# Kernel tuning notes

Measured on AMD Instinct MI355X. Metric: run time of the kernel, lower is better.

## Reference

```python
import jax, jax.numpy as jnp
import numpy as np
import math

D_MODEL = 1024
H = 16
D_K = D_MODEL // H
D_FF = 4096
NEG = -1e9


def layer_norm(x, alpha, bias):
    # Faithful to source: mean over last dim, UNBIASED std (torch.std default),
    # eps defined in source but never used in forward.
    mean = jnp.mean(x, axis=-1, keepdims=True)
    std = jnp.std(x, axis=-1, ddof=1, keepdims=True)
    return (x - mean) / std * alpha + bias


def mha(x, mask, w_q, w_k, w_v, w_o):
    B, S, D = x.shape
    q = (x @ w_q.T).reshape(B, S, H, D_K)
    k = (x @ w_k.T).reshape(B, S, H, D_K)
    v = (x @ w_v.T).reshape(B, S, H, D_K)
    scores = jnp.einsum('bqhd,bkhd->bhqk', q, k) / math.sqrt(D_K)
    scores = jnp.where(mask, NEG, scores)
    attn = jax.nn.softmax(scores, axis=-1)
    out = jnp.einsum('bhqk,bkhd->bqhd', attn, v).reshape(B, S, D)
    return out @ w_o.T


def setup_inputs() -> dict:
    key = jax.random.key(0)
    ks = jax.random.split(key, 16)
    B, S = 4, 2048
    s = 0.02
    return {
        'x': jax.random.normal(ks[0], (B, S, D_MODEL), jnp.float32),
        'w_q': jax.random.normal(ks[1], (D_MODEL, D_MODEL), jnp.float32) * s,
        'w_k': jax.random.normal(ks[2], (D_MODEL, D_MODEL), jnp.float32) * s,
        'w_v': jax.random.normal(ks[3], (D_MODEL, D_MODEL), jnp.float32) * s,
        'w_o': jax.random.normal(ks[4], (D_MODEL, D_MODEL), jnp.float32) * s,
        'l1_w': jax.random.normal(ks[5], (D_FF, D_MODEL), jnp.float32) * s,
        'l1_b': jnp.zeros((D_FF,), jnp.float32),
        'l2_w': jax.random.normal(ks[6], (D_MODEL, D_FF), jnp.float32) * s,
        'l2_b': jnp.zeros((D_MODEL,), jnp.float32),
        'norm1_a': jnp.ones((D_MODEL,), jnp.float32),
        'norm1_b': jnp.zeros((D_MODEL,), jnp.float32),
        'norm2_a': jnp.ones((D_MODEL,), jnp.float32),
        'norm2_b': jnp.zeros((D_MODEL,), jnp.float32),
        'normf_a': jnp.ones((D_MODEL,), jnp.float32),
        'normf_b': jnp.zeros((D_MODEL,), jnp.float32),
        'mask': jax.random.randint(ks[7], (B, 1, 1, S), 0, 2) == 1,
    }


def reference(x, w_q, w_k, w_v, w_o, l1_w, l1_b, l2_w, l2_b,
              norm1_a, norm1_b, norm2_a, norm2_b, normf_a, normf_b, mask):
    # residual 1: pre-norm self-attention (dropout is identity at eval)
    x = x + mha(layer_norm(x, norm1_a, norm1_b), mask, w_q, w_k, w_v, w_o)
    # residual 2: pre-norm FFN
    h = layer_norm(x, norm2_a, norm2_b)
    ff = jax.nn.relu(h @ l1_w.T + l1_b) @ l2_w.T + l2_b
    x = x + ff
    return layer_norm(x, normf_a, normf_b)
```

## Files before the change

### kernel.cpp

```cpp
#include <hip/hip_runtime.h>
#include <hip/hip_bf16.h>


typedef __bf16 bf16x8 __attribute__((ext_vector_type(8)));
typedef float f32x4 __attribute__((ext_vector_type(4)));
typedef unsigned short u16x8 __attribute__((ext_vector_type(8)));
using bf16 = __hip_bfloat16;

__device__ __forceinline__ f32x4 mfma16(bf16x8 a, bf16x8 b, f32x4 c) {
  return __builtin_amdgcn_mfma_f32_16x16x32_bf16(a, b, c, 0, 0, 0);
}

__device__ __forceinline__ int swz(int row, int blk) {
  return row * 64 + ((blk ^ (row & 7)) << 3);
}

__device__ __forceinline__ void stage_tile64(unsigned short* lds,
                                             const bf16* g, int ld, int rows) {
  const int lane = threadIdx.x & 63, wid = threadIdx.x >> 6;
  const int r8 = lane >> 3, blk = lane & 7;
  const bf16* gl = g + (size_t)r8 * ld + ((blk ^ r8) << 3);
  const int passes = rows >> 3;
  for (int p = wid; p < passes; p += 4) {
    __builtin_amdgcn_global_load_lds(
        (const __attribute__((address_space(1))) void*)(gl + (size_t)(p * 8) * ld),
        (__attribute__((address_space(3))) void*)(lds + p * 512),
        16, 0, 0);
  }
}

__device__ __forceinline__ void stage_half512(unsigned short* lds,
                                              const bf16* g, int ld) {
  const int lane = threadIdx.x & 63, w8 = threadIdx.x >> 6;
  const int r8 = lane >> 3, blk = lane & 7;
  const bf16* gl = g + (size_t)r8 * ld + ((blk ^ r8) << 3);
  __builtin_amdgcn_global_load_lds(
      (const __attribute__((address_space(1))) void*)(gl + (size_t)(w8 * 8) * ld),
      (__attribute__((address_space(3))) void*)(lds + w8 * 512), 16, 0, 0);
  __builtin_amdgcn_global_load_lds(
      (const __attribute__((address_space(1))) void*)(gl + (size_t)((w8 + 8) * 8) * ld),
      (__attribute__((address_space(3))) void*)(lds + (w8 + 8) * 512), 16, 0, 0);
}

__device__ __forceinline__ short bfb(float x) {
  return (short)__hip_bfloat16_raw(__float2bfloat16(x)).x;
}

__global__ __launch_bounds__(256) void cvt_k(const float* __restrict__ s,
                                             bf16* __restrict__ d, int n) {
  const int i = (blockIdx.x * 256 + threadIdx.x) * 4;
  if (i + 3 < n) {
    const float4 v = *reinterpret_cast<const float4*>(s + i);
    ushort4 o;
    o.x = (unsigned short)bfb(v.x);
    o.y = (unsigned short)bfb(v.y);
    o.z = (unsigned short)bfb(v.z);
    o.w = (unsigned short)bfb(v.w);
    *reinterpret_cast<ushort4*>(d + i) = o;
  }
}

template <bool OUT_F32>
__global__ __launch_bounds__(256) void layernorm_k(const float* __restrict__ in,
                                                   const float* __restrict__ gamma,
                                                   const float* __restrict__ beta,
                                                   void* __restrict__ out) {
  __shared__ float red[8];
  const int row = blockIdx.x, t = threadIdx.x;
  const float4 vv = reinterpret_cast<const float4*>(in + (size_t)row * 1024)[t];
  const float x0 = vv.x, x1 = vv.y, x2 = vv.z, x3 = vv.w;
  float s = x0 + x1 + x2 + x3;
#pragma unroll
  for (int off = 32; off; off >>= 1) s += __shfl_down(s, off);
  if ((t & 63) == 0) red[t >> 6] = s;
  __syncthreads();
  const float mean = (red[0] + red[1] + red[2] + red[3]) * (1.0f / 1024.0f);
  const float d0 = x0 - mean, d1 = x1 - mean, d2 = x2 - mean, d3 = x3 - mean;
  float sq = d0 * d0 + d1 * d1 + d2 * d2 + d3 * d3;
#pragma unroll
  for (int off = 32; off; off >>= 1) sq += __shfl_down(sq, off);
  if ((t & 63) == 0) red[4 + (t >> 6)] = sq;
  __syncthreads();
  const float var =
      fmaxf((red[4] + red[5] + red[6] + red[7]) * (1.0f / 1023.0f), 1e-20f);
  const float rstd = rsqrtf(var);
  const float4 ga = reinterpret_cast<const float4*>(gamma)[t];
  const float4 be = reinterpret_cast<const float4*>(beta)[t];
  const float y0 = d0 * rstd * ga.x + be.x;
  const float y1 = d1 * rstd * ga.y + be.y;
  const float y2 = d2 * rstd * ga.z + be.z;
  const float y3 = d3 * rstd * ga.w + be.w;
  if (OUT_F32) {
    reinterpret_cast<float4*>((float*)out + (size_t)row * 1024)[t] =
        make_float4(y0, y1, y2, y3);
  } else {
    ushort4 o;
    o.x = (unsigned short)bfb(y0);
    o.y = (unsigned short)bfb(y1);
    o.z = (unsigned short)bfb(y2);
    o.w = (unsigned short)bfb(y3);
    reinterpret_cast<ushort4*>((bf16*)out + (size_t)row * 1024)[t] = o;
  }
}

template <bool HAS_BIAS, bool RELU, bool HAS_RES, bool OUT_F32>
__global__ __launch_bounds__(256) void gemm_bt(const bf16* __restrict__ A,
                                               const bf16* __restrict__ W,
                                               const float* __restrict__ bias,
                                               const float* __restrict__ resid,
                                               void* __restrict__ out,
                                               int M, int N, int K,
                                               int lda, int ldw) {
  __shared__ __align__(16) unsigned short As[128 * 64];
  __shared__ __align__(16) unsigned short Bs[128 * 64];
  const int lane = threadIdx.x & 63, wid = threadIdx.x >> 6;
  const int n16 = lane & 15, quad = lane >> 4;
  const int wm = (wid >> 1) * 64, wn = (wid & 1) * 64;
  const int tm = blockIdx.x * 128, tn = blockIdx.y * 128;
  f32x4 acc[4][4] = {};
  for (int k0 = 0; k0 < K; k0 += 64) {
    stage_tile64(As, A + (size_t)tm * lda + k0, lda, 128);
    stage_tile64(Bs, W + (size_t)tn * ldw + k0, ldw, 128);
    __syncthreads();
#pragma unroll
    for (int kk = 0; kk < 64; kk += 32) {
      bf16x8 af[4], bw[4];
#pragma unroll
      for (int i = 0; i < 4; ++i)
        af[i] = *reinterpret_cast<const bf16x8*>(
            &As[swz(wm + i * 16 + n16, (kk >> 3) + quad)]);
#pragma unroll
      for (int j = 0; j < 4; ++j)
        bw[j] = *reinterpret_cast<const bf16x8*>(
            &Bs[swz(wn + j * 16 + n16, (kk >> 3) + quad)]);
#pragma unroll
      for (int i = 0; i < 4; ++i)
#pragma unroll
        for (int j = 0; j < 4; ++j) acc[i][j] = mfma16(af[i], bw[j], acc[i][j]);
    }
    __syncthreads();
  }
#pragma unroll
  for (int i = 0; i < 4; ++i) {
#pragma unroll
    for (int j = 0; j < 4; ++j) {
      const int n = tn + wn + j * 16 + n16;
      const float bv = HAS_BIAS ? bias[n] : 0.0f;
#pragma unroll
      for (int r = 0; r < 4; ++r) {
        const int m = tm + wm + i * 16 + quad * 4 + r;
        float vv = acc[i][j][r] + bv;
        if (RELU) vv = fmaxf(vv, 0.0f);
        if (HAS_RES) vv += resid[(size_t)m * N + n];
        if (OUT_F32)
          ((float*)out)[(size_t)m * N + n] = vv;
        else
          ((bf16*)out)[(size_t)m * N + n] = __float2bfloat16(vv);
      }
    }
  }
}

#define PHASE2(BUFSEL, QB, DO_B, STAGES, WAITS)                                \
  {                                                                            \
    const unsigned short* LA = Lds + (BUFSEL)*32768 + lasel * 8192;            \
    if (DO_B) {                                                                \
      const unsigned short* LB =                                               \
          Lds + (BUFSEL)*32768 + 16384 + lbsel * 8192;                         \
      _Pragma("unroll") for (int j = 0; j < 4; ++j) {                          \
        const int br = bloc + j * 16 + n16;                                    \
        bfr[j][0] = *reinterpret_cast<const bf16x8*>(&LB[swz(br, quad)]);      \
        bfr[j][1] = *reinterpret_cast<const bf16x8*>(&LB[swz(br, 4 + quad)]);  \
      }                                                                        \
    }                                                                          \
    bf16x8 a0[4], a1[4];                                                       \
    _Pragma("unroll") for (int ii = 0; ii < 4; ++ii) {                         \
      const int ar = ((QB)*2 + ii) * 16 + n16;                                 \
      a0[ii] = *reinterpret_cast<const bf16x8*>(&LA[swz(ar, quad)]);           \
      a1[ii] = *reinterpret_cast<const bf16x8*>(&LA[swz(ar, 4 + quad)]);       \
    }                                                                          \
    STAGES;                                                                    \
    WAITS;                                                                     \
    __builtin_amdgcn_sched_barrier(0);                                         \
    __builtin_amdgcn_s_barrier();                                              \
    asm volatile("s_waitcnt lgkmcnt(0)" ::: "memory");                         \
    __builtin_amdgcn_sched_barrier(0);                                         \
    __builtin_amdgcn_s_setprio(1);                                             \
    _Pragma("unroll") for (int ii = 0; ii < 4; ++ii)                           \
        _Pragma("unroll") for (int j = 0; j < 4; ++j) {                        \
      f32x4 c = acc[(QB)*2 + ii][j];                                           \
      c = mfma16(a0[ii], bfr[j][0], c);                                        \
      c = mfma16(a1[ii], bfr[j][1], c);                                        \
      acc[(QB)*2 + ii][j] = c;                                                 \
    }                                                                          \
    __builtin_amdgcn_s_setprio(0);                                             \
    __builtin_amdgcn_sched_barrier(0);                                         \
    __builtin_amdgcn_s_barrier();                                              \
  }

template <bool QKV, bool HAS_BIAS, bool RELU>
__global__ __launch_bounds__(512, 2) void gemm256_k(
    const bf16* __restrict__ A0p, const bf16* __restrict__ cln,
    const bf16* __restrict__ W, const float* __restrict__ bias,
    const int* __restrict__ cnt, bf16* __restrict__ out,
    bf16* __restrict__ kvout, int M, int N, int K, int lda, int ldw) {
  __shared__ __align__(16) unsigned short Lds[65536];
  const int tm = blockIdx.x * 256;
  const int tn = blockIdx.y * 256;
  const bf16* A = A0p;
  bool isQ = true;
  if (QKV) {
    isQ = (blockIdx.y < 4);
    if (!isQ) {
      const int npad = (cnt[tm >> 11] + 127) & ~127;
      if ((tm & 2047) >= npad) return;
      A = cln;
    }
  }
  const int lane = threadIdx.x & 63, w8 = threadIdx.x >> 6;
  const int n16 = lane & 15, quad = lane >> 4;
  const int wm = (w8 >> 2) << 7;
  const int wn = (w8 & 3) << 6;
  const int lasel = wm >> 7, lbsel = wn >> 7, bloc = wn & 127;
  const int NTT = K >> 6;
  const bf16* Ag = A + (size_t)tm * lda;
  const bf16* Wg = W + (size_t)tn * ldw;
  f32x4 acc[8][4] = {};

  auto STAGE = [&](int bufsel, int region, int tile) {
    unsigned short* dst = Lds + bufsel * 32768 + region * 8192;
    if (region < 2)
      stage_half512(dst, Ag + (size_t)(region * 128) * lda + tile * 64, lda);
    else
      stage_half512(dst, Wg + (size_t)((region - 2) * 128) * ldw + tile * 64,
                    ldw);
  };

  STAGE(0, 0, 0); STAGE(0, 1, 0); STAGE(0, 2, 0); STAGE(0, 3, 0);
  STAGE(1, 2, 1); STAGE(1, 3, 1);
  asm volatile("s_waitcnt vmcnt(4)" ::: "memory");
  __builtin_amdgcn_sched_barrier(0);
  __builtin_amdgcn_s_barrier();

  for (int i = 0; i < NTT; i += 2) {
    const bool hasNext = (i + 2 < NTT);
    bf16x8 bfr[4][2];
    PHASE2(0, 0, true, { STAGE(1, 0, i + 1); STAGE(1, 1, i + 1); }, );
    PHASE2(0, 2, false,
           if (hasNext) { STAGE(0, 2, i + 2); STAGE(0, 3, i + 2); },
           if (hasNext) { asm volatile("s_waitcnt vmcnt(4)" ::: "memory"); }
           else { asm volatile("s_waitcnt vmcnt(0)" ::: "memory"); });
    PHASE2(1, 0, true,
           if (hasNext) { STAGE(0, 0, i + 2); STAGE(0, 1, i + 2); }, );
    PHASE2(1, 2, false,
           if (hasNext && i + 3 < NTT) { STAGE(1, 2, i + 3); STAGE(1, 3, i + 3); },
           if (hasNext) { asm volatile("s_waitcnt vmcnt(4)" ::: "memory"); });
  }
  bf16* op;
  int ldo, nc0;
  if (QKV && !isQ) {
    op = kvout; ldo = 2048; nc0 = tn - 1024;
  } else if (QKV) {
    op = out; ldo = 1024; nc0 = tn;
  } else {
    op = out; ldo = N; nc0 = tn;
  }
#pragma unroll
  for (int i = 0; i < 8; ++i) {
#pragma unroll
    for (int j = 0; j < 4; ++j) {
      const int n = nc0 + wn + j * 16 + n16;
      const float bv = HAS_BIAS ? bias[n] : 0.0f;
#pragma unroll
      for (int r = 0; r < 4; ++r) {
        const int m = tm + wm + i * 16 + quad * 4 + r;
        float vv = acc[i][j][r] + bv;
        if (RELU) vv = fmaxf(vv, 0.0f);
        op[(size_t)m * ldo + n] = __float2bfloat16(vv);
      }
    }
  }
}

__global__ __launch_bounds__(256) void prep_mask_k(const int* __restrict__ m,
                                                   float* __restrict__ mf,
                                                   int n) {
  __shared__ int s;
  if (threadIdx.x == 0) s = 0;
  __syncthreads();
  unsigned int acc = 0;
  for (int i = threadIdx.x; i < 512; i += 256)
    acc |= ((const unsigned int*)m)[i] & 0xFFFFFF00u;
  if (acc) atomicOr(&s, 1);
  __syncthreads();
  const bool bytes = (s != 0);
  const int i = blockIdx.x * 256 + threadIdx.x;
  if (i < n) {
    const int v = bytes ? (int)((const unsigned char*)m)[i] : m[i];
    mf[i] = v ? -1.4427e9f : 0.0f;
  }
}

__global__ __launch_bounds__(256) void scan_k(const float* __restrict__ maskf,
                                              float* __restrict__ cmask,
                                              int* __restrict__ idx,
                                              int* __restrict__ cnt) {
  __shared__ int wsum[4];
  const int b = blockIdx.x, t = threadIdx.x, lane = t & 63, w = t >> 6;
  const float* mrow = maskf + b * 2048;
  int keep[8], local = 0;
#pragma unroll
  for (int e = 0; e < 8; ++e) {
    keep[e] = (mrow[t * 8 + e] == 0.0f) ? 1 : 0;
    local += keep[e];
  }
  int inc = local;
#pragma unroll
  for (int off = 1; off < 64; off <<= 1) {
    int v = __shfl_up(inc, off);
    if (lane >= off) inc += v;
  }
  if (lane == 63) wsum[w] = inc;
  __syncthreads();
  int base = 0;
#pragma unroll
  for (int i = 0; i < 4; ++i)
    if (i < w) base += wsum[i];
  int p = base + inc - local;
#pragma unroll
  for (int e = 0; e < 8; ++e)
    if (keep[e]) idx[b * 2048 + p++] = t * 8 + e;
  const int total = wsum[0] + wsum[1] + wsum[2] + wsum[3];
  if (t == 0) cnt[b] = total;
  for (int i = t; i < 2048; i += 256)
    cmask[b * 2048 + i] = (i < total) ? 0.0f : -1.4427e9f;
}

__global__ __launch_bounds__(128) void gatherA_k(const bf16* __restrict__ ln1,
                                                 const int* __restrict__ idx,
                                                 const int* __restrict__ cnt,
                                                 bf16* __restrict__ cln) {
  const int b = blockIdx.x >> 11, j = blockIdx.x & 2047;
  const int n = cnt[b];
  const int npad = (n + 127) & ~127;
  if (j >= npad) return;
  u16x8* dst = reinterpret_cast<u16x8*>(cln + ((size_t)(b * 2048 + j)) * 1024);
  if (j < n) {
    const int s = idx[b * 2048 + j];
    const u16x8* src =
        reinterpret_cast<const u16x8*>(ln1 + ((size_t)(b * 2048 + s)) * 1024);
    dst[threadIdx.x] = src[threadIdx.x];
  } else {
    u16x8 z = {};
    dst[threadIdx.x] = z;
  }
}

__global__ __launch_bounds__(256) void attn_k(const bf16* __restrict__ q,
                                              const bf16* __restrict__ kv,
                                              const float* __restrict__ cmask,
                                              const int* __restrict__ cnt,
                                              bf16* __restrict__ out, int BHN) {
  __shared__ __align__(16) unsigned short Ks[2][64 * 64];
  __shared__ __align__(16) unsigned short Vs[2][64 * 72];
  const int lane = threadIdx.x & 63, wid = threadIdx.x >> 6;
  const int n16 = lane & 15, quad = lane >> 4;
  const int bid0 = blockIdx.x;
  const int nwg = gridDim.x;
  const int bid = (bid0 & 7) * (nwg >> 3) + (bid0 >> 3);
  const int qb = bid & 15, bh = bid >> 4;
  const int b = bh >> 4, h = bh & 15;
  const bf16* qp0 = q + (size_t)b * 2048 * 1024 + h * 64;
  const bf16* kp0 = kv + (size_t)b * 2048 * 2048 + h * 64;
  const bf16* vp0 = kp0 + 1024;
  const float* mfb = cmask + b * 2048;
  const int cntb = cnt[b];
  const int nk = ((cntb + 63) >> 6) << 6;
  const int qrow0 = qb * 128 + wid * 32;

  bf16x8 qf[2][2];
#pragma unroll
  for (int g = 0; g < 2; ++g) {
    const bf16* qp = qp0 + (size_t)(qrow0 + g * 16 + n16) * 1024 + quad * 8;
    qf[g][0] = *reinterpret_cast<const bf16x8*>(qp);
    qf[g][1] = *reinterpret_cast<const bf16x8*>(qp + 32);
  }
  bf16x8 ones;
#pragma unroll
  for (int e = 0; e < 8; ++e) ones[e] = (__bf16)1.0f;
  f32x4 oacc[2][4] = {};
  f32x4 lacc[2] = {};
  const int prow = ((n16 >> 2) << 3) + (n16 & 3);
  const int vkey = lane, vdc = wid * 16;

  stage_tile64(Ks[0], kp0, 2048, 64);
  {
    const bf16* vp = vp0 + (size_t)vkey * 2048 + vdc;
    const u16x8 a = *reinterpret_cast<const u16x8*>(vp);
    const u16x8 bq = *reinterpret_cast<const u16x8*>(vp + 8);
#pragma unroll
    for (int e = 0; e < 8; ++e) {
      Vs[0][(vdc + e) * 72 + vkey] = a[e];
      Vs[0][(vdc + 8 + e) * 72 + vkey] = bq[e];
    }
  }
  int cur = 0;
  for (int kt = 0; kt < nk; kt += 64) {
    __syncthreads();
    const bool hasNext = (kt + 64 < nk);
    const bool fullTile = (kt + 64 <= cntb);
    u16x8 na = {}, nb = {};
    if (hasNext) {
      stage_tile64(Ks[cur ^ 1], kp0 + (size_t)(kt + 64) * 2048, 2048, 64);
      const bf16* vp = vp0 + (size_t)(kt + 64 + vkey) * 2048 + vdc;
      na = *reinterpret_cast<const u16x8*>(vp);
      nb = *reinterpret_cast<const u16x8*>(vp + 8);
    }
    const unsigned short* Kc = Ks[cur];
    const unsigned short* Vc = Vs[cur];
#pragma unroll
    for (int sub = 0; sub < 2; ++sub) {
      const int kb = sub * 32;
      bf16x8 aflo[2], afhi[2];
#pragma unroll
      for (int st = 0; st < 2; ++st) {
        const int row = kb + prow + st * 4;
        aflo[st] = *reinterpret_cast<const bf16x8*>(&Kc[swz(row, quad)]);
        afhi[st] = *reinterpret_cast<const bf16x8*>(&Kc[swz(row, 4 + quad)]);
      }
      __builtin_amdgcn_s_setprio(1);
      f32x4 z[2][2];
#pragma unroll
      for (int g = 0; g < 2; ++g)
#pragma unroll
        for (int st = 0; st < 2; ++st) {
          f32x4 zz = {};
          zz = mfma16(aflo[st], qf[g][0], zz);
          zz = mfma16(afhi[st], qf[g][1], zz);
          z[g][st] = zz;
        }
      __builtin_amdgcn_s_setprio(0);
      float4 m0 = make_float4(0.f, 0.f, 0.f, 0.f);
      float4 m1 = make_float4(0.f, 0.f, 0.f, 0.f);
      if (!fullTile) {
        m0 = *reinterpret_cast<const float4*>(mfb + kt + kb + quad * 8);
        m1 = *reinterpret_cast<const float4*>(mfb + kt + kb + quad * 8 + 4);
      }
      bf16x8 vf[4];
#pragma unroll
      for (int j = 0; j < 4; ++j)
        vf[j] = *reinterpret_cast<const bf16x8*>(
            &Vc[(j * 16 + n16) * 72 + kb + quad * 8]);
#pragma unroll
      for (int g = 0; g < 2; ++g) {
        bf16x8 pf;
#pragma unroll
        for (int r = 0; r < 4; ++r) {
          const float e0 = __builtin_amdgcn_exp2f(
              fmaf(z[g][0][r], 0.18033688f, ((const float*)&m0)[r]));
          const float e1 = __builtin_amdgcn_exp2f(
              fmaf(z[g][1][r], 0.18033688f, ((const float*)&m1)[r]));
          pf[r] = (__bf16)e0;
          pf[4 + r] = (__bf16)e1;
        }
        __builtin_amdgcn_s_setprio(1);
#pragma unroll
        for (int j = 0; j < 4; ++j) oacc[g][j] = mfma16(pf, vf[j], oacc[g][j]);
        lacc[g] = mfma16(pf, ones, lacc[g]);
        __builtin_amdgcn_s_setprio(0);
      }
    }
    if (hasNext) {
      unsigned short* Vn = Vs[cur ^ 1];
#pragma unroll
      for (int e = 0; e < 8; ++e) {
        Vn[(vdc + e) * 72 + vkey] = na[e];
        Vn[(vdc + 8 + e) * 72 + vkey] = nb[e];
      }
    }
    cur ^= 1;
  }
#pragma unroll
  for (int g = 0; g < 2; ++g) {
#pragma unroll
    for (int r = 0; r < 4; ++r) {
      const float lr = 1.0f / fmaxf(lacc[g][r], 1e-20f);
      bf16* op =
          out + (size_t)(b * 2048 + qrow0 + g * 16 + quad * 4 + r) * 1024 +
          h * 64;
#pragma unroll
      for (int j = 0; j < 4; ++j)
        op[j * 16 + n16] = __float2bfloat16(oacc[g][j][r] * lr);
    }
  }
}

extern "C" void kernel_launch(void* const* d_in, const int* in_sizes, int n_in,
                              void* d_out, int out_size, void* d_ws,
                              size_t ws_size, hipStream_t stream) {
  const float* x    = (const float*)d_in[0];
  const float* w_q  = (const float*)d_in[1];
  const float* w_k  = (const float*)d_in[2];
  const float* w_v  = (const float*)d_in[3];
  const float* w_o  = (const float*)d_in[4];
  const float* l1_w = (const float*)d_in[5];
  const float* l1_b = (const float*)d_in[6];
  const float* l2_w = (const float*)d_in[7];
  const float* l2_b = (const float*)d_in[8];
  const float* n1a  = (const float*)d_in[9];
  const float* n1b  = (const float*)d_in[10];
  const float* n2a  = (const float*)d_in[11];
  const float* n2b  = (const float*)d_in[12];
  const float* nfa  = (const float*)d_in[13];
  const float* nfb  = (const float*)d_in[14];
  const int* mask   = (const int*)d_in[15];

  const int D = 1024, FF = 4096;
  const int M = in_sizes[0] / D;
  const int B = M / 2048;

  const size_t MB = 1024ull * 1024ull;
  if (ws_size < 121 * MB) return;
  char* w = (char*)d_ws;
  bf16* WQKV = (bf16*)(w + 0 * MB);
  bf16* WO   = (bf16*)(w + 6 * MB);
  bf16* L1W  = (bf16*)(w + 8 * MB);
  bf16* L2W  = (bf16*)(w + 16 * MB);
  bf16* LN1  = (bf16*)(w + 24 * MB);
  bf16* Qbuf = (bf16*)(w + 40 * MB);
  bf16* ATT  = LN1;
  bf16* HLN  = (bf16*)(w + 40 * MB);
  bf16* CLN  = (bf16*)(w + 56 * MB);
  bf16* FF1  = (bf16*)(w + 56 * MB);
  bf16* KV   = (bf16*)(w + 88 * MB);
  float* X1  = (float*)(w + 88 * MB);
  float* MASKF = (float*)(w + 120 * MB);
  float* CMASK = (float*)(w + 120 * MB + 256 * 1024);
  int*   IDX   = (int*)(w + 120 * MB + 512 * 1024);
  int*   CNT   = (int*)(w + 120 * MB + 768 * 1024);

  const dim3 blk(256);
  cvt_k<<<dim3(D * D / 1024), blk, 0, stream>>>(w_q, WQKV, D * D);
  cvt_k<<<dim3(D * D / 1024), blk, 0, stream>>>(w_k, WQKV + D * D, D * D);
  cvt_k<<<dim3(D * D / 1024), blk, 0, stream>>>(w_v, WQKV + 2 * D * D, D * D);
  cvt_k<<<dim3(D * D / 1024), blk, 0, stream>>>(w_o, WO, D * D);
  cvt_k<<<dim3(FF * D / 1024), blk, 0, stream>>>(l1_w, L1W, FF * D);
  cvt_k<<<dim3(FF * D / 1024), blk, 0, stream>>>(l2_w, L2W, FF * D);
  prep_mask_k<<<dim3((M + 255) / 256), blk, 0, stream>>>(mask, MASKF, M);
  scan_k<<<dim3(B), blk, 0, stream>>>(MASKF, CMASK, IDX, CNT);

  layernorm_k<false><<<M, blk, 0, stream>>>(x, n1a, n1b, LN1);
  gatherA_k<<<dim3(B * 2048), dim3(128), 0, stream>>>(LN1, IDX, CNT, CLN);
  gemm256_k<true, false, false><<<dim3(M / 256, 12), dim3(512), 0, stream>>>(
      LN1, CLN, WQKV, nullptr, CNT, Qbuf, KV, M, 3072, 1024, 1024, 1024);
  const int BHN = B * 16;
  attn_k<<<dim3((M / 128) * 16), blk, 0, stream>>>(Qbuf, KV, CMASK, CNT, ATT,
                                                   BHN);
  gemm_bt<false, false, true, true><<<dim3(M / 128, D / 128), blk, 0, stream>>>(
      ATT, WO, nullptr, x, X1, M, D, D, D, D);
  layernorm_k<false><<<M, blk, 0, stream>>>(X1, n2a, n2b, HLN);
  for (int c = 0; c < 2; ++c) {
    gemm256_k<false, true, true><<<dim3(M / 256, 8), dim3(512), 0, stream>>>(
        HLN, nullptr, L1W + (size_t)c * 2048 * D, l1_b + c * 2048, nullptr,
        FF1, nullptr, M, 2048, 1024, 1024, 1024);
    if (c == 0)
      gemm_bt<true, false, true, true>
          <<<dim3(M / 128, D / 128), blk, 0, stream>>>(
              FF1, L2W + c * 2048, l2_b, X1, X1, M, D, 2048, 2048, FF);
    else
      gemm_bt<false, false, true, true>
          <<<dim3(M / 128, D / 128), blk, 0, stream>>>(
              FF1, L2W + c * 2048, nullptr, X1, X1, M, D, 2048, 2048, FF);
  }
  layernorm_k<true><<<M, blk, 0, stream>>>(X1, nfa, nfb, (float*)d_out);
}
```

Baseline: 504.8 us.

## Triple-buffer A tiles in 256 GEMM and fuse weight conversions into one launch

The 256x256 GEMM now keeps three rotating LDS slots for A tiles and two for B tiles (160 KB of LDS), so loads for tiles i+2 and i+3 are issued earlier and deeper prefetch can hide global latency. Because of the larger LDS footprint, launch bounds drop from two blocks per CU to one, which reduces occupancy. Separately, the six weight fp32-to-bf16 conversion launches are merged into a single kernel that picks its source by block index, removing per-launch overhead.

After: 493.4 us. 2.2% less time.

```diff
diff --git a/kernel.cpp b/kernel.cpp
--- a/kernel.cpp
+++ b/kernel.cpp
@@ -46,18 +46,37 @@
   return (short)__hip_bfloat16_raw(__float2bfloat16(x)).x;
 }
 
-__global__ __launch_bounds__(256) void cvt_k(const float* __restrict__ s,
-                                             bf16* __restrict__ d, int n) {
-  const int i = (blockIdx.x * 256 + threadIdx.x) * 4;
-  if (i + 3 < n) {
-    const float4 v = *reinterpret_cast<const float4*>(s + i);
-    ushort4 o;
-    o.x = (unsigned short)bfb(v.x);
-    o.y = (unsigned short)bfb(v.y);
-    o.z = (unsigned short)bfb(v.z);
-    o.w = (unsigned short)bfb(v.w);
-    *reinterpret_cast<ushort4*>(d + i) = o;
-  }
+__global__ __launch_bounds__(256) void cvt_all_k(
+    const float* __restrict__ wq, const float* __restrict__ wk,
+    const float* __restrict__ wv, const float* __restrict__ wo,
+    const float* __restrict__ l1, const float* __restrict__ l2,
+    bf16* __restrict__ WQKV, bf16* __restrict__ WO, bf16* __restrict__ L1W,
+    bf16* __restrict__ L2W) {
+  const int bid = blockIdx.x;
+  const float* s;
+  bf16* d;
+  int lb;
+  if (bid < 1024) {
+    s = wq; d = WQKV; lb = bid;
+  } else if (bid < 2048) {
+    s = wk; d = WQKV + (1 << 20); lb = bid - 1024;
+  } else if (bid < 3072) {
+    s = wv; d = WQKV + (2 << 20); lb = bid - 2048;
+  } else if (bid < 4096) {
+    s = wo; d = WO; lb = bid - 3072;
+  } else if (bid < 8192) {
+    s = l1; d = L1W; lb = bid - 4096;
+  } else {
+    s = l2; d = L2W; lb = bid - 8192;
+  }
+  const int i = lb * 1024 + threadIdx.x * 4;
+  const float4 v = *reinterpret_cast<const float4*>(s + i);
+  ushort4 o;
+  o.x = (unsigned short)bfb(v.x);
+  o.y = (unsigned short)bfb(v.y);
+  o.z = (unsigned short)bfb(v.z);
+  o.w = (unsigned short)bfb(v.w);
+  *reinterpret_cast<ushort4*>(d + i) = o;
 }
 
 template <bool OUT_F32>
@@ -161,12 +180,11 @@
   }
 }
 
-#define PHASE2(BUFSEL, QB, DO_B, STAGES, WAITS)                                \
+#define PHASE3(LAB, LBB, QB, DO_B, STAGES, WAITS)                              \
   {                                                                            \
-    const unsigned short* LA = Lds + (BUFSEL)*32768 + lasel * 8192;            \
+    const unsigned short* LA = (LAB) + lasel * 8192;                           \
     if (DO_B) {                                                                \
-      const unsigned short* LB =                                               \
-          Lds + (BUFSEL)*32768 + 16384 + lbsel * 8192;                         \
+      const unsigned short* LB = (LBB) + lbsel * 8192;                         \
       _Pragma("unroll") for (int j = 0; j < 4; ++j) {                          \
         const int br = bloc + j * 16 + n16;                                    \
         bfr[j][0] = *reinterpret_cast<const bf16x8*>(&LB[swz(br, quad)]);      \
@@ -199,12 +217,12 @@
   }
 
 template <bool QKV, bool HAS_BIAS, bool RELU>
-__global__ __launch_bounds__(512, 2) void gemm256_k(
+__global__ __launch_bounds__(512, 1) void gemm256_k(
     const bf16* __restrict__ A0p, const bf16* __restrict__ cln,
     const bf16* __restrict__ W, const float* __restrict__ bias,
     const int* __restrict__ cnt, bf16* __restrict__ out,
     bf16* __restrict__ kvout, int M, int N, int K, int lda, int ldw) {
-  __shared__ __align__(16) unsigned short Lds[65536];
+  __shared__ __align__(16) unsigned short Lds[81920];
   const int tm = blockIdx.x * 256;
   const int tn = blockIdx.y * 256;
   const bf16* A = A0p;
@@ -227,34 +245,41 @@
   const bf16* Wg = W + (size_t)tn * ldw;
   f32x4 acc[8][4] = {};
 
-  auto STAGE = [&](int bufsel, int region, int tile) {
-    unsigned short* dst = Lds + bufsel * 32768 + region * 8192;
-    if (region < 2)
-      stage_half512(dst, Ag + (size_t)(region * 128) * lda + tile * 64, lda);
-    else
-      stage_half512(dst, Wg + (size_t)((region - 2) * 128) * ldw + tile * 64,
-                    ldw);
+  auto STAGEA = [&](int slot, int tile) {
+    unsigned short* dst = Lds + slot * 16384;
+    stage_half512(dst, Ag + tile * 64, lda);
+    stage_half512(dst + 8192, Ag + (size_t)128 * lda + tile * 64, lda);
   };
-
-  STAGE(0, 0, 0); STAGE(0, 1, 0); STAGE(0, 2, 0); STAGE(0, 3, 0);
-  STAGE(1, 2, 1); STAGE(1, 3, 1);
-  asm volatile("s_waitcnt vmcnt(4)" ::: "memory");
+  auto STAGEB = [&](int slot, int tile) {
+    unsigned short* dst = Lds + 49152 + slot * 16384;
+    stage_half512(dst, Wg + tile * 64, ldw);
+    stage_half512(dst + 8192, Wg + (size_t)128 * ldw + tile * 64, ldw);
+  };
+
+  STAGEA(0, 0); STAGEB(0, 0);
+  STAGEA(1, 1); STAGEB(1, 1);
+  asm volatile("s_waitcnt vmcnt(8)" ::: "memory");
   __builtin_amdgcn_sched_barrier(0);
   __builtin_amdgcn_s_barrier();
 
+  int sA = 0;
   for (int i = 0; i < NTT; i += 2) {
     const bool hasNext = (i + 2 < NTT);
+    const int sA1 = (sA + 1 == 3) ? 0 : sA + 1;
+    const int sA2 = (sA1 + 1 == 3) ? 0 : sA1 + 1;
+    const unsigned short* LAi = Lds + sA * 16384;
+    const unsigned short* LAi1 = Lds + sA1 * 16384;
+    const unsigned short* LB0 = Lds + 49152;
+    const unsigned short* LB1 = Lds + 49152 + 16384;
     bf16x8 bfr[4][2];
-    PHASE2(0, 0, true, { STAGE(1, 0, i + 1); STAGE(1, 1, i + 1); }, );
-    PHASE2(0, 2, false,
-           if (hasNext) { STAGE(0, 2, i + 2); STAGE(0, 3, i + 2); },
-           if (hasNext) { asm volatile("s_waitcnt vmcnt(4)" ::: "memory"); }
+    PHASE3(LAi, LB0, 0, true, if (hasNext) STAGEA(sA2, i + 2), );
+    PHASE3(LAi, LB0, 2, false, if (hasNext) STAGEB(0, i + 2),
+           if (hasNext) { asm volatile("s_waitcnt vmcnt(8)" ::: "memory"); }
            else { asm volatile("s_waitcnt vmcnt(0)" ::: "memory"); });
-    PHASE2(1, 0, true,
-           if (hasNext) { STAGE(0, 0, i + 2); STAGE(0, 1, i + 2); }, );
-    PHASE2(1, 2, false,
-           if (hasNext && i + 3 < NTT) { STAGE(1, 2, i + 3); STAGE(1, 3, i + 3); },
-           if (hasNext) { asm volatile("s_waitcnt vmcnt(4)" ::: "memory"); });
+    PHASE3(LAi1, LB1, 0, true, if (hasNext) STAGEA(sA, i + 3), );
+    PHASE3(LAi1, LB1, 2, false, if (hasNext) STAGEB(1, i + 3),
+           if (hasNext) { asm volatile("s_waitcnt vmcnt(8)" ::: "memory"); });
+    sA = sA2;
   }
   bf16* op;
   int ldo, nc0;
@@ -540,12 +565,8 @@
   int*   CNT   = (int*)(w + 120 * MB + 768 * 1024);
 
   const dim3 blk(256);
-  cvt_k<<<dim3(D * D / 1024), blk, 0, stream>>>(w_q, WQKV, D * D);
-  cvt_k<<<dim3(D * D / 1024), blk, 0, stream>>>(w_k, WQKV + D * D, D * D);
-  cvt_k<<<dim3(D * D / 1024), blk, 0, stream>>>(w_v, WQKV + 2 * D * D, D * D);
-  cvt_k<<<dim3(D * D / 1024), blk, 0, stream>>>(w_o, WO, D * D);
-  cvt_k<<<dim3(FF * D / 1024), blk, 0, stream>>>(l1_w, L1W, FF * D);
-  cvt_k<<<dim3(FF * D / 1024), blk, 0, stream>>>(l2_w, L2W, FF * D);
+  cvt_all_k<<<dim3(12288), blk, 0, stream>>>(w_q, w_k, w_v, w_o, l1_w, l2_w,
+                                             WQKV, WO, L1W, L2W);
   prep_mask_k<<<dim3((M + 255) / 256), blk, 0, stream>>>(mask, MASKF, M);
   scan_k<<<dim3(B), blk, 0, stream>>>(MASKF, CMASK, IDX, CNT);
 
```
